# Kernel optimization log

Hardware: AMD Instinct MI355X
Metric: run time of the kernel (lower is better)

The kernel has to match this reference:

```python
import jax, jax.numpy as jnp
import numpy as np

NUM_EMBEDDINGS = 1024
DIM_EMBEDDING = 256
COMMITMENT_COST = 0.25


def setup_inputs() -> dict:
    key = jax.random.key(0)
    k1, k2 = jax.random.split(key)
    inputs = jax.random.normal(k1, (64, DIM_EMBEDDING, 32, 32), dtype=jnp.float32)
    # torch init: uniform(-1/K, 1/K)
    w = jax.random.uniform(k2, (NUM_EMBEDDINGS, DIM_EMBEDDING), dtype=jnp.float32,
                           minval=-1.0 / NUM_EMBEDDINGS, maxval=1.0 / NUM_EMBEDDINGS)
    return {"inputs": inputs, "w": w}


def reference(inputs, w):
    # NCHW -> NHWC
    x = jnp.transpose(inputs, (0, 2, 3, 1))            # [B,H,W,D]
    input_shape = x.shape
    flat = x.reshape(-1, DIM_EMBEDDING)                # [N,D]

    distances = (jnp.sum(flat * flat, axis=1, keepdims=True)
                 - 2.0 * jnp.matmul(flat, w.T)
                 + jnp.sum(w * w, axis=1))

    encoding_indices = jnp.argmax(-distances, axis=1)[:, None]      # [N,1] int
    encodings = jax.nn.one_hot(encoding_indices[:, 0], NUM_EMBEDDINGS,
                               dtype=jnp.float32)                   # [N,K]

    # gather instead of one-hot matmul (same math)
    quantized = jnp.take(w, encoding_indices[:, 0], axis=0)          # [N,D]
    quantized = quantized.reshape(input_shape)                       # [B,H,W,D]

    e_latent_loss = jnp.mean((jax.lax.stop_gradient(quantized) - x) ** 2)
    q_latent_loss = jnp.mean((quantized - jax.lax.stop_gradient(x)) ** 2)
    vq_loss = q_latent_loss + COMMITMENT_COST * e_latent_loss

    # straight-through estimator
    quantized_st = x + jax.lax.stop_gradient(quantized - x)
    quantized_out = jnp.transpose(quantized_st, (0, 3, 1, 2))        # NHWC -> NCHW

    avg_probs = jnp.mean(encodings, axis=0)
    perplexity = jnp.exp(-jnp.sum(avg_probs * jnp.log(avg_probs + 1e-10)))

    return (distances, quantized_out, vq_loss, encodings, encoding_indices, perplexity)
```

## Files before the change

kernel.cpp:

```cpp
#include <hip/hip_runtime.h>
#include <hip/hip_fp16.h>

#define N_TOT   65536
#define K_EMB   1024
#define D_EMB   256
#define HW      1024
#define CHW     (D_EMB * HW)

#define O_DIST  0
#define O_Q     67108864
#define O_LOSS  83886080
#define O_ENC   83886081
#define O_IDX   150994945
#define O_PPL   151060481

#define WS_CNT   0
#define WS_LOSSP 4096
#define WS_XX    12288
#define WS_WW    274432
#define WS_AIDX  278528

#define CAP     15
#define MARGIN  3.0e-4f

typedef float  f32x4  __attribute__((ext_vector_type(4)));
typedef short  short8 __attribute__((ext_vector_type(8)));
typedef unsigned short ushort8 __attribute__((ext_vector_type(8)));
typedef f32x4 __attribute__((aligned(4))) f32x4u;

static __device__ __forceinline__ void gload16(const void* g, void* l) {
  __builtin_amdgcn_global_load_lds(
      (const __attribute__((address_space(1))) unsigned int*)g,
      (__attribute__((address_space(3))) unsigned int*)l, 16, 0, 0);
}

__global__ __launch_bounds__(256) void k_prep_x(const float* __restrict__ in,
                                                unsigned short* __restrict__ x2,
                                                float* __restrict__ xx) {
  int n = blockIdx.x * 256 + threadIdx.x;
  int b = n >> 10, hw = n & 1023;
  const float* p = in + (size_t)b * CHW + hw;
  float hsum[2];
  #pragma unroll
  for (int half = 0; half < 2; ++half) {
    float r[8];
    for (int i = 0; i < 128; i += 8) {
      ushort8 hv;
      #pragma unroll
      for (int j = 0; j < 8; ++j) {
        int d = half * 128 + i + j;
        float v = p[(size_t)d * HW];
        float sq = v * v;
        asm volatile("" : "+v"(sq));
        if (i == 0) r[j] = sq; else r[j] += sq;
        hv[j] = __half_as_ushort(__float2half_rn(v));
      }
      *(ushort8*)&x2[(size_t)n * 256 + half * 128 + i] = hv;
    }
    hsum[half] = ((r[0] + r[1]) + (r[2] + r[3])) + ((r[4] + r[5]) + (r[6] + r[7]));
  }
  xx[n] = hsum[0] + hsum[1];
}

__global__ __launch_bounds__(256) void k_prep_w(const float* __restrict__ w,
                                                unsigned short* __restrict__ w2,
                                                float* __restrict__ ww) {
  int k = blockIdx.x * 256 + threadIdx.x;
  const float* p = w + (size_t)k * D_EMB;
  float hsum[2];
  #pragma unroll
  for (int half = 0; half < 2; ++half) {
    float r[8];
    for (int i = 0; i < 128; i += 8) {
      ushort8 hv;
      #pragma unroll
      for (int j = 0; j < 8; ++j) {
        float v = p[half * 128 + i + j];
        float sq = v * v;
        asm volatile("" : "+v"(sq));
        if (i == 0) r[j] = sq; else r[j] += sq;
        hv[j] = __half_as_ushort(__float2half_rn(v * 1024.f));
      }
      *(ushort8*)&w2[(size_t)k * 256 + half * 128 + i] = hv;
    }
    hsum[half] = ((r[0] + r[1]) + (r[2] + r[3])) + ((r[4] + r[5]) + (r[6] + r[7]));
  }
  ww[k] = hsum[0] + hsum[1];
}

__global__ __launch_bounds__(512) void k_coarse(const unsigned short* __restrict__ x2,
                                                const unsigned short* __restrict__ w2,
                                                const float* __restrict__ xx,
                                                const float* __restrict__ ww,
                                                float* __restrict__ dist,
                                                unsigned short* __restrict__ cand) {
  __shared__ __align__(16) short As[2][4096];
  __shared__ __align__(16) short Bs[2][4096];
  __shared__ unsigned rowprov[128];
  __shared__ unsigned rowcnt[128];
  __shared__ unsigned short rowcand[128][CAP];

  const int tid = threadIdx.x;
  const int l = tid & 63, v = tid >> 6;
  const int n0 = blockIdx.x * 128;
  const int qr = v >> 1, qc = v & 1;

  if (tid < 128) { rowprov[tid] = 0x7F800000u; rowcnt[tid] = 0u; }

  float xv[2][4];
  #pragma unroll
  for (int m = 0; m < 2; ++m)
    #pragma unroll
    for (int r = 0; r < 4; ++r)
      xv[m][r] = xx[n0 + qr * 32 + m * 16 + (l >> 4) * 4 + r];

  const int srcrow = tid >> 2, srcoff = (tid & 3) * 16;

  #define STAGE(buf, u) do {                                                   \
    int k0_ = ((u) >> 3) * 128, d0_ = ((u) & 7) * 32;                          \
    gload16((const char*)x2 + (size_t)(n0 + srcrow) * 512 + d0_ * 2 + srcoff,  \
            (char*)As[buf] + v * 1024);                                        \
    gload16((const char*)w2 + (size_t)(k0_ + srcrow) * 512 + d0_ * 2 + srcoff, \
            (char*)Bs[buf] + v * 1024);                                        \
  } while (0)

  f32x4 acc[2][4];
  int cur = 0;
  STAGE(0, 0);
  __syncthreads();

  for (int u = 0; u < 64; ++u) {
    if ((u & 7) == 0) {
      #pragma unroll
      for (int m = 0; m < 2; ++m)
        #pragma unroll
        for (int n = 0; n < 4; ++n) acc[m][n] = (f32x4){0.f, 0.f, 0.f, 0.f};
    }
    if (u < 63) STAGE(cur ^ 1, u + 1);

    short8 af[2], bfr[4];
    #pragma unroll
    for (int m = 0; m < 2; ++m)
      af[m] = *(const short8*)((const char*)As[cur] +
                               (qr * 32 + m * 16 + (l & 15)) * 64 + (l >> 4) * 16);
    #pragma unroll
    for (int n = 0; n < 4; ++n)
      bfr[n] = *(const short8*)((const char*)Bs[cur] +
                                (qc * 64 + n * 16 + (l & 15)) * 64 + (l >> 4) * 16);
    #pragma unroll
    for (int m = 0; m < 2; ++m)
      #pragma unroll
      for (int n = 0; n < 4; ++n)
        asm("v_mfma_f32_16x16x32_f16 %0, %1, %2, %0"
            : "+v"(acc[m][n]) : "v"(af[m]), "v"(bfr[n]));

    if ((u & 7) == 7) {
      const int k0 = (u >> 3) * 128;
      float wv[4];
      float rmin[2][4];
      #pragma unroll
      for (int m = 0; m < 2; ++m)
        #pragma unroll
        for (int r = 0; r < 4; ++r) rmin[m][r] = 3.4e38f;
      #pragma unroll
      for (int n = 0; n < 4; ++n) {
        const int kg = k0 + qc * 64 + n * 16 + (l & 15);
        wv[n] = ww[kg];
        #pragma unroll
        for (int m = 0; m < 2; ++m)
          #pragma unroll
          for (int r = 0; r < 4; ++r) {
            const int rl = qr * 32 + m * 16 + (l >> 4) * 4 + r;
            float dd = (xv[m][r] - acc[m][n][r] * (1.f / 512.f)) + wv[n];
            dist[(size_t)(n0 + rl) * 1024 + kg] = dd;
            rmin[m][r] = fminf(rmin[m][r], dd);
          }
      }
      #pragma unroll
      for (int off = 1; off < 16; off <<= 1)
        #pragma unroll
        for (int m = 0; m < 2; ++m)
          #pragma unroll
          for (int r = 0; r < 4; ++r)
            rmin[m][r] = fminf(rmin[m][r], __shfl_xor(rmin[m][r], off));
      if ((l & 15) == 0) {
        #pragma unroll
        for (int m = 0; m < 2; ++m)
          #pragma unroll
          for (int r = 0; r < 4; ++r)
            atomicMin(&rowprov[qr * 32 + m * 16 + (l >> 4) * 4 + r],
                      __float_as_uint(rmin[m][r]));
      }
      __syncthreads();
      #pragma unroll
      for (int n = 0; n < 4; ++n) {
        const int kg = k0 + qc * 64 + n * 16 + (l & 15);
        #pragma unroll
        for (int m = 0; m < 2; ++m)
          #pragma unroll
          for (int r = 0; r < 4; ++r) {
            const int rl = qr * 32 + m * 16 + (l >> 4) * 4 + r;
            float dd = (xv[m][r] - acc[m][n][r] * (1.f / 512.f)) + wv[n];
            if (dd < __uint_as_float(rowprov[rl]) + MARGIN) {
              unsigned slot = atomicAdd(&rowcnt[rl], 1u);
              if (slot < CAP) rowcand[rl][slot] = (unsigned short)kg;
            }
          }
      }
    }
    __syncthreads();
    cur ^= 1;
  }

  if (tid < 128) {
    unsigned c = rowcnt[tid];
    unsigned short* dst = cand + (size_t)(n0 + tid) * 16;
    dst[0] = (c > CAP) ? (unsigned short)0xFFFF : (unsigned short)c;
    #pragma unroll
    for (int i = 0; i < CAP; ++i) dst[1 + i] = rowcand[tid][i];
  }
  #undef STAGE
}

__global__ __launch_bounds__(256) void k_reeval(const float* __restrict__ in,
                                                const float* __restrict__ w,
                                                const float* __restrict__ xx,
                                                const float* __restrict__ ww,
                                                const unsigned short* __restrict__ cand,
                                                int* __restrict__ aidx) {
  int n = blockIdx.x * 256 + threadIdx.x;
  int b = n >> 10, hw = n & 1023;
  const unsigned short* c = cand + (size_t)n * 16;
  int cnt = c[0];
  int best;
  if (cnt == 1) {
    best = c[1];
  } else {
    const float* xp = in + (size_t)b * CHW + hw;
    const float xxv = xx[n];
    float bd = 3.4e38f; int bk = 1 << 30;
    const bool full = (cnt > CAP);
    const int m = full ? K_EMB : cnt;
    for (int i = 0; i < m; ++i) {
      int k = full ? i : (int)c[1 + i];
      const float* wr = w + (size_t)k * D_EMB;
      float acc = 0.f;
      for (int d = 0; d < D_EMB; ++d)
        acc = fmaf(xp[(size_t)d * HW], wr[d], acc);
      float t = 2.0f * acc;
      asm volatile("" : "+v"(t));
      float s = xxv - t;
      asm volatile("" : "+v"(s));
      float dd = s + ww[k];
      if (dd < bd || (dd == bd && k < bk)) { bd = dd; bk = k; }
    }
    best = bk;
  }
  aidx[n] = best;
}

__global__ __launch_bounds__(256) void k_epi2(const float* __restrict__ in,
                                              const float* __restrict__ w,
                                              const int* __restrict__ aidx,
                                              float* __restrict__ outq,
                                              float* __restrict__ enc,
                                              float* __restrict__ idxf,
                                              int* __restrict__ cnt,
                                              double* __restrict__ lossp) {
  __shared__ double sred[256];
  __shared__ int sidx[64];
  const int tid = threadIdx.x;
  const int rr = tid & 63, qd = tid >> 6;
  const int n0 = blockIdx.x * 64;
  const int n = n0 + rr;
  const int b = n >> 10, hw = n & 1023;
  if (qd == 0) sidx[rr] = aidx[n];
  __syncthreads();
  const int idx = sidx[rr];
  const float* xp = in + (size_t)b * CHW + hw;
  float* qp = outq + (size_t)b * CHW + hw;
  const float* wrow = w + (size_t)idx * D_EMB;
  double ls = 0.0;
  for (int j = 0; j < 64; ++j) {
    int d = qd * 64 + j;
    float xvv = xp[(size_t)d * HW];
    float q = wrow[d];
    float t = q - xvv;
    qp[(size_t)d * HW] = xvv + t;
    ls += (double)(t * t);
  }
  if (qd == 0) { idxf[n] = (float)idx; atomicAdd(&cnt[idx], 1); }
  for (int it = 0; it < 64; ++it) {
    int ii = sidx[it];
    f32x4 z = {0.f, 0.f, 0.f, 0.f};
    if ((ii >> 2) == tid) z[ii & 3] = 1.f;
    *(f32x4u*)&enc[(size_t)(n0 + it) * 1024 + tid * 4] = z;
  }
  sred[tid] = ls; __syncthreads();
  for (int s = 128; s > 0; s >>= 1) {
    if (tid < s) sred[tid] += sred[tid + s];
    __syncthreads();
  }
  if (tid == 0) lossp[blockIdx.x] = sred[0];
}

__global__ __launch_bounds__(256) void k_final(const double* __restrict__ lossp,
                                               const int* __restrict__ cnt,
                                               float* __restrict__ out_loss,
                                               float* __restrict__ out_ppl) {
  __shared__ double sred[256];
  int t = threadIdx.x;
  sred[t] = lossp[t] + lossp[t + 256] + lossp[t + 512] + lossp[t + 768];
  __syncthreads();
  for (int s = 128; s > 0; s >>= 1) {
    if (t < s) sred[t] += sred[t + s];
    __syncthreads();
  }
  if (t == 0) *out_loss = (float)(1.25 * (sred[0] / 16777216.0));
  __syncthreads();
  double es = 0.0;
  for (int k = t; k < K_EMB; k += 256) {
    float p = (float)cnt[k] * (1.0f / 65536.0f);
    float term = p * logf(p + 1e-10f);
    es += (double)term;
  }
  sred[t] = es;
  __syncthreads();
  for (int s = 128; s > 0; s >>= 1) {
    if (t < s) sred[t] += sred[t + s];
    __syncthreads();
  }
  if (t == 0) *out_ppl = expf((float)(-sred[0]));
}

extern "C" void kernel_launch(void* const* d_in, const int* in_sizes, int n_in,
                              void* d_out, int out_size, void* d_ws, size_t ws_size,
                              hipStream_t stream) {
  const float* in = (const float*)d_in[0];
  const float* w  = (const float*)d_in[1];
  float* out = (float*)d_out;
  char* ws = (char*)d_ws;

  int*    cnt   = (int*)(ws + WS_CNT);
  double* lossp = (double*)(ws + WS_LOSSP);
  float*  xx    = (float*)(ws + WS_XX);
  float*  wwp   = (float*)(ws + WS_WW);
  int*    aidx  = (int*)(ws + WS_AIDX);

  unsigned short* x2   = (unsigned short*)(out + O_ENC + 3);
  unsigned short* w2   = x2 + (size_t)N_TOT * 256;
  unsigned short* cand = w2 + (size_t)K_EMB * 256;

  hipMemsetAsync(cnt, 0, 4096, stream);

  k_prep_x<<<256, 256, 0, stream>>>(in, x2, xx);
  k_prep_w<<<4, 256, 0, stream>>>(w, w2, wwp);
  k_coarse<<<512, 512, 0, stream>>>(x2, w2, xx, wwp, out + O_DIST, cand);
  k_reeval<<<256, 256, 0, stream>>>(in, w, xx, wwp, cand, aidx);
  k_epi2<<<1024, 256, 0, stream>>>(in, w, aidx, out + O_Q, out + O_ENC,
                                   out + O_IDX, cnt, lossp);
  k_final<<<1, 256, 0, stream>>>(lossp, cnt, out + O_LOSS, out + O_PPL);
}
```

Measured before the change: 1.027 ms.

## Swizzle MFMA LDS tiles and split epilogue into coalesced quantize and encoding kernels

Applies an XOR swizzle to the LDS staging and fragment reads of the coarse MFMA kernel to reduce bank conflicts. The quantize epilogue is restructured so each block handles one batch and an 8-channel slice. It stages that slice of the codebook in padded shared memory and does float4 coalesced reads and writes of the NCHW tensors instead of per-row strided gathers. The one-hot encoding write moves to its own kernel, and the index and count outputs move into the re-evaluation kernel. This adds a kernel launch and enlarges the loss partial buffer.

```diff
diff --git a/kernel.cpp b/kernel.cpp
--- a/kernel.cpp
+++ b/kernel.cpp
@@ -16,9 +16,9 @@
 
 #define WS_CNT   0
 #define WS_LOSSP 4096
-#define WS_XX    12288
-#define WS_WW    274432
-#define WS_AIDX  278528
+#define WS_XX    20480
+#define WS_WW    282624
+#define WS_AIDX  286720
 
 #define CAP     15
 #define MARGIN  3.0e-4f
@@ -27,6 +27,8 @@
 typedef short  short8 __attribute__((ext_vector_type(8)));
 typedef unsigned short ushort8 __attribute__((ext_vector_type(8)));
 typedef f32x4 __attribute__((aligned(4))) f32x4u;
+
+#define SWZ(row) ((((row) & 3) ^ (((row) >> 2) & 1)) << 4)
 
 static __device__ __forceinline__ void gload16(const void* g, void* l) {
   __builtin_amdgcn_global_load_lds(
@@ -114,7 +116,8 @@
     for (int r = 0; r < 4; ++r)
       xv[m][r] = xx[n0 + qr * 32 + m * 16 + (l >> 4) * 4 + r];
 
-  const int srcrow = tid >> 2, srcoff = (tid & 3) * 16;
+  const int srcrow = tid >> 2;
+  const int srcoff = ((tid & 3) * 16) ^ SWZ(srcrow);
 
   #define STAGE(buf, u) do {                                                   \
     int k0_ = ((u) >> 3) * 128, d0_ = ((u) & 7) * 32;                          \
@@ -140,13 +143,17 @@
 
     short8 af[2], bfr[4];
     #pragma unroll
-    for (int m = 0; m < 2; ++m)
+    for (int m = 0; m < 2; ++m) {
+      int row = qr * 32 + m * 16 + (l & 15);
       af[m] = *(const short8*)((const char*)As[cur] +
-                               (qr * 32 + m * 16 + (l & 15)) * 64 + (l >> 4) * 16);
-    #pragma unroll
-    for (int n = 0; n < 4; ++n)
+                               row * 64 + (((l >> 4) * 16) ^ SWZ(row)));
+    }
+    #pragma unroll
+    for (int n = 0; n < 4; ++n) {
+      int row = qc * 64 + n * 16 + (l & 15);
       bfr[n] = *(const short8*)((const char*)Bs[cur] +
-                                (qc * 64 + n * 16 + (l & 15)) * 64 + (l >> 4) * 16);
+                                row * 64 + (((l >> 4) * 16) ^ SWZ(row)));
+    }
     #pragma unroll
     for (int m = 0; m < 2; ++m)
       #pragma unroll
@@ -227,20 +234,22 @@
                                                 const float* __restrict__ xx,
                                                 const float* __restrict__ ww,
                                                 const unsigned short* __restrict__ cand,
-                                                int* __restrict__ aidx) {
+                                                int* __restrict__ aidx,
+                                                float* __restrict__ idxf,
+                                                int* __restrict__ cnt) {
   int n = blockIdx.x * 256 + threadIdx.x;
   int b = n >> 10, hw = n & 1023;
   const unsigned short* c = cand + (size_t)n * 16;
-  int cnt = c[0];
+  int cc = c[0];
   int best;
-  if (cnt == 1) {
+  if (cc == 1) {
     best = c[1];
   } else {
     const float* xp = in + (size_t)b * CHW + hw;
     const float xxv = xx[n];
     float bd = 3.4e38f; int bk = 1 << 30;
-    const bool full = (cnt > CAP);
-    const int m = full ? K_EMB : cnt;
+    const bool full = (cc > CAP);
+    const int m = full ? K_EMB : cc;
     for (int i = 0; i < m; ++i) {
       int k = full ? i : (int)c[1 + i];
       const float* wr = w + (size_t)k * D_EMB;
@@ -257,51 +266,70 @@
     best = bk;
   }
   aidx[n] = best;
+  idxf[n] = (float)best;
+  atomicAdd(&cnt[best], 1);
 }
 
 __global__ __launch_bounds__(256) void k_epi2(const float* __restrict__ in,
                                               const float* __restrict__ w,
                                               const int* __restrict__ aidx,
                                               float* __restrict__ outq,
-                                              float* __restrict__ enc,
-                                              float* __restrict__ idxf,
-                                              int* __restrict__ cnt,
                                               double* __restrict__ lossp) {
+  __shared__ float wsub[1024 * 9];
+  __shared__ int sidx[1024];
   __shared__ double sred[256];
+  const int tid = threadIdx.x;
+  const int b = blockIdx.x >> 5, dg = blockIdx.x & 31;
+  const int d0 = dg * 8;
+  for (int it = 0; it < 32; ++it) {
+    int kk = it * 32 + (tid >> 3);
+    int cc = tid & 7;
+    wsub[kk * 9 + cc] = w[(size_t)kk * D_EMB + d0 + cc];
+  }
+  { f32x4 z;
+    const int4 iv = *(const int4*)&aidx[b * 1024 + tid * 4];
+    sidx[tid * 4 + 0] = iv.x; sidx[tid * 4 + 1] = iv.y;
+    sidx[tid * 4 + 2] = iv.z; sidx[tid * 4 + 3] = iv.w; (void)z; }
+  __syncthreads();
+  const int hw4 = tid * 4;
+  const int i0 = sidx[hw4], i1 = sidx[hw4 + 1], i2 = sidx[hw4 + 2], i3 = sidx[hw4 + 3];
+  const float* ip = in + (size_t)b * CHW + hw4;
+  float* qp = outq + (size_t)b * CHW + hw4;
+  double ls = 0.0;
+  #pragma unroll
+  for (int dd = 0; dd < 8; ++dd) {
+    const int d = d0 + dd;
+    float4 xv = *(const float4*)&ip[(size_t)d * HW];
+    float q0 = wsub[i0 * 9 + dd], q1 = wsub[i1 * 9 + dd];
+    float q2 = wsub[i2 * 9 + dd], q3 = wsub[i3 * 9 + dd];
+    float t0 = q0 - xv.x, t1 = q1 - xv.y, t2 = q2 - xv.z, t3 = q3 - xv.w;
+    float4 o;
+    o.x = xv.x + t0; o.y = xv.y + t1; o.z = xv.z + t2; o.w = xv.w + t3;
+    *(float4*)&qp[(size_t)d * HW] = o;
+    ls += (double)(t0 * t0) + (double)(t1 * t1)
+        + (double)(t2 * t2) + (double)(t3 * t3);
+  }
+  sred[tid] = ls; __syncthreads();
+  for (int s = 128; s > 0; s >>= 1) {
+    if (tid < s) sred[tid] += sred[tid + s];
+    __syncthreads();
+  }
+  if (tid == 0) lossp[blockIdx.x] = sred[0];
+}
+
+__global__ __launch_bounds__(256) void k_enc(const int* __restrict__ aidx,
+                                             float* __restrict__ enc) {
   __shared__ int sidx[64];
   const int tid = threadIdx.x;
-  const int rr = tid & 63, qd = tid >> 6;
   const int n0 = blockIdx.x * 64;
-  const int n = n0 + rr;
-  const int b = n >> 10, hw = n & 1023;
-  if (qd == 0) sidx[rr] = aidx[n];
-  __syncthreads();
-  const int idx = sidx[rr];
-  const float* xp = in + (size_t)b * CHW + hw;
-  float* qp = outq + (size_t)b * CHW + hw;
-  const float* wrow = w + (size_t)idx * D_EMB;
-  double ls = 0.0;
-  for (int j = 0; j < 64; ++j) {
-    int d = qd * 64 + j;
-    float xvv = xp[(size_t)d * HW];
-    float q = wrow[d];
-    float t = q - xvv;
-    qp[(size_t)d * HW] = xvv + t;
-    ls += (double)(t * t);
-  }
-  if (qd == 0) { idxf[n] = (float)idx; atomicAdd(&cnt[idx], 1); }
+  if (tid < 64) sidx[tid] = aidx[n0 + tid];
+  __syncthreads();
   for (int it = 0; it < 64; ++it) {
     int ii = sidx[it];
     f32x4 z = {0.f, 0.f, 0.f, 0.f};
     if ((ii >> 2) == tid) z[ii & 3] = 1.f;
     *(f32x4u*)&enc[(size_t)(n0 + it) * 1024 + tid * 4] = z;
   }
-  sred[tid] = ls; __syncthreads();
-  for (int s = 128; s > 0; s >>= 1) {
-    if (tid < s) sred[tid] += sred[tid + s];
-    __syncthreads();
-  }
-  if (tid == 0) lossp[blockIdx.x] = sred[0];
 }
 
 __global__ __launch_bounds__(256) void k_final(const double* __restrict__ lossp,
@@ -310,7 +338,10 @@
                                                float* __restrict__ out_ppl) {
   __shared__ double sred[256];
   int t = threadIdx.x;
-  sred[t] = lossp[t] + lossp[t + 256] + lossp[t + 512] + lossp[t + 768];
+  double a = 0.0;
+  #pragma unroll
+  for (int i = 0; i < 8; ++i) a += lossp[t + 256 * i];
+  sred[t] = a;
   __syncthreads();
   for (int s = 128; s > 0; s >>= 1) {
     if (t < s) sred[t] += sred[t + s];
@@ -356,8 +387,9 @@
   k_prep_x<<<256, 256, 0, stream>>>(in, x2, xx);
   k_prep_w<<<4, 256, 0, stream>>>(w, w2, wwp);
   k_coarse<<<512, 512, 0, stream>>>(x2, w2, xx, wwp, out + O_DIST, cand);
-  k_reeval<<<256, 256, 0, stream>>>(in, w, xx, wwp, cand, aidx);
-  k_epi2<<<1024, 256, 0, stream>>>(in, w, aidx, out + O_Q, out + O_ENC,
-                                   out + O_IDX, cnt, lossp);
+  k_reeval<<<256, 256, 0, stream>>>(in, w, xx, wwp, cand, aidx,
+                                    out + O_IDX, cnt);
+  k_epi2<<<2048, 256, 0, stream>>>(in, w, aidx, out + O_Q, lossp);
+  k_enc<<<1024, 256, 0, stream>>>(aidx, out + O_ENC);
   k_final<<<1, 256, 0, stream>>>(lossp, cnt, out + O_LOSS, out + O_PPL);
 }
```

Result: no change. 1.020 ms (-0.7%).
